# Optimization experiments

Measured on AMD Instinct MI355X. Metric: run time of the kernel, lower is better.

The kernel has to match this reference:

```python
import jax, jax.numpy as jnp
import numpy as np

N = 50000
E = 800000
C_IN = 32
C_OUT = 32
K = 8  # number of branch MLPs


def setup_inputs() -> dict:
    key = jax.random.key(0)
    ks = jax.random.split(key, 12)
    x = jax.random.normal(ks[0], (N, C_IN), dtype=jnp.float32)
    pos = jax.random.normal(ks[1], (N, 2), dtype=jnp.float32)
    edge_index = jax.random.randint(ks[2], (2, E), 0, N, dtype=jnp.int32)
    edge_attr = jax.random.normal(ks[3], (E, 4), dtype=jnp.float32)
    edge_weight = jax.random.uniform(ks[4], (E,), dtype=jnp.float32)
    s1 = 1.0 / np.sqrt(C_IN + 4)
    s2 = 1.0 / np.sqrt(C_OUT)
    W1 = jax.random.uniform(ks[5], (K, C_IN + 4, C_OUT), jnp.float32, -s1, s1)
    b1 = jax.random.uniform(ks[6], (K, C_OUT), jnp.float32, -s1, s1)
    W2 = jax.random.uniform(ks[7], (K, C_OUT, C_OUT), jnp.float32, -s2, s2)
    b2 = jax.random.uniform(ks[8], (K, C_OUT), jnp.float32, -s2, s2)
    sr = 1.0 / np.sqrt(C_IN)
    Wr = jax.random.uniform(ks[9], (C_IN, C_OUT), jnp.float32, -sr, sr)
    br = jax.random.uniform(ks[10], (C_OUT,), jnp.float32, -sr, sr)
    return {"x": x, "pos": pos, "edge_index": edge_index, "edge_attr": edge_attr,
            "edge_weight": edge_weight, "W1": W1, "b1": b1, "W2": W2, "b2": b2,
            "Wr": Wr, "br": br}


def reference(x, pos, edge_index, edge_attr, edge_weight, W1, b1, W2, b2, Wr, br):
    src = edge_index[0]  # j (source / neighbor)
    tgt = edge_index[1]  # i (target / aggregation index)

    # gather per-edge features
    x_i = x[tgt]                      # [E, C_IN]
    x_j = x[src]                      # [E, C_IN]
    diff = pos[src] - pos[tgt]        # [E, 2]

    # geometric branch index in [0, 8)
    con0 = (diff[:, 0] > 0).astype(jnp.int32)
    con1 = (diff[:, 1] > 0).astype(jnp.int32)
    con2 = (jnp.abs(diff[:, 0]) - jnp.abs(diff[:, 1]) > 0).astype(jnp.int32)
    idx = con0 + con1 * 2 + con2 * 4  # [E]

    m = jnp.concatenate([x_j - x_i, edge_attr], axis=1)  # [E, C_IN+4]
    # all 8 branch MLPs (Linear->ReLU->Linear->ReLU), then select per edge
    h = jax.nn.relu(jnp.einsum('ec,kcf->ekf', m, W1) + b1[None])   # [E, K, C_OUT]
    f_all = jax.nn.relu(jnp.einsum('ekf,kfg->ekg', h, W2) + b2[None])
    f = jnp.take_along_axis(f_all, idx[:, None, None], axis=1)[:, 0, :]  # [E, C_OUT]
    f = edge_weight[:, None] * f

    # scatter-mean over target nodes
    seg_sum = jax.ops.segment_sum(f, tgt, num_segments=N)
    counts = jax.ops.segment_sum(jnp.ones((f.shape[0],), f.dtype), tgt, num_segments=N)
    out = seg_sum / jnp.maximum(counts, 1.0)[:, None]

    # skip connection
    out = out + x @ Wr + br
    return out
```

## Files before the change

kernel.cpp:

```cpp
#include <hip/hip_runtime.h>

#define N_NODES 50000
#define N_EDGES 800000
#define K_BR    8
#define N_C     196
#define N_BUK   1568
#define CAP_SLOTS 898816
#define MLP_WAVES (CAP_SLOTS/64)
#define FATB    98

typedef _Float16 h2 __attribute__((ext_vector_type(2)));
typedef _Float16 half8 __attribute__((ext_vector_type(8)));
typedef float f32x4 __attribute__((ext_vector_type(4)));

#define MFMA(a, b, c) __builtin_amdgcn_mfma_f32_16x16x32_f16((a), (b), (c), 0, 0, 0)


__device__ __forceinline__ int branch_idx(float dx, float dy) {
    return (dx > 0.0f ? 1 : 0) + (dy > 0.0f ? 2 : 0) +
           ((fabsf(dx) - fabsf(dy)) > 0.0f ? 4 : 0);
}

__device__ __forceinline__ unsigned pk_f16pair(float a, float b) {
    h2 p; p.x = (_Float16)a; p.y = (_Float16)b;
    return __builtin_bit_cast(unsigned, p);
}

__device__ __forceinline__ unsigned short f16bits(float a) {
    _Float16 h = (_Float16)a;
    return __builtin_bit_cast(unsigned short, h);
}

__global__ void __launch_bounds__(1024) hist_kernel(
    const int* __restrict__ ei, const float* __restrict__ pos,
    const float* __restrict__ x,
    int* __restrict__ bucketCnt, unsigned short* __restrict__ kcArr,
    unsigned* __restrict__ xh) {
    __shared__ int h[N_BUK];
    int t = threadIdx.x;
    for (int j = t; j < N_BUK; j += 1024) h[j] = 0;
    __syncthreads();
#pragma unroll
    for (int i = 0; i < 8; ++i) {
        int e = blockIdx.x * 8192 + i * 1024 + t;
        if (e < N_EDGES) {
            int s = ei[e], d = ei[N_EDGES + e];
            float2 ps = ((const float2*)pos)[s];
            float2 pd = ((const float2*)pos)[d];
            int k = branch_idx(ps.x - pd.x, ps.y - pd.y);
            int b = k * N_C + (d >> 8);
            atomicAdd(&h[b], 1);
            kcArr[e] = (unsigned short)b;
            float2 xv = ((const float2*)x)[e];
            xh[e] = pk_f16pair(xv.x, xv.y);
        }
    }
    __syncthreads();
    for (int j = t; j < N_BUK; j += 1024) {
        int c = h[j];
        if (c) atomicAdd(&bucketCnt[j], c);
    }
}

__global__ void __launch_bounds__(1024) tiny_kernel(
    const int* __restrict__ bucketCnt, int* __restrict__ slotStart,
    int* __restrict__ binStart,
    const float* __restrict__ W1, const float* __restrict__ W2,
    uint4* __restrict__ w1f4, uint4* __restrict__ w2f4) {
    __shared__ int sc[1024];
    __shared__ int sb[256];
    int t = threadIdx.x;
    int b0 = 2 * t, b1 = 2 * t + 1;
    int a0 = (b0 < N_BUK) ? ((bucketCnt[b0] + 63) & ~63) : 0;
    int a1 = (b1 < N_BUK) ? ((bucketCnt[b1] + 63) & ~63) : 0;
    sc[t] = a0 + a1;
    __syncthreads();
    for (int off = 1; off < 1024; off <<= 1) {
        int tmp = (t >= off) ? sc[t - off] : 0;
        __syncthreads();
        sc[t] += tmp;
        __syncthreads();
    }
    int excl = sc[t] - (a0 + a1);
    if (b0 < N_BUK) slotStart[b0] = excl;
    if (b1 < N_BUK) slotStart[b1] = excl + a0;
    if (t == 1023) slotStart[N_BUK] = sc[1023];

    int v = 0;
    if (t < N_C) {
#pragma unroll
        for (int k = 0; k < K_BR; ++k) v += bucketCnt[k * N_C + t];
    }
    if (t < 256) sb[t] = v;
    __syncthreads();
    for (int off = 1; off < 256; off <<= 1) {
        int tmp = (t < 256 && t >= off) ? sb[t - off] : 0;
        __syncthreads();
        if (t < 256) sb[t] += tmp;
        __syncthreads();
    }
    if (t < N_C) binStart[t] = sb[t] - v;
    if (t == 255) binStart[N_C] = sb[255];

    for (int idx = t; idx < 3072; idx += 1024) {
        if (idx < 2048) {
            int L = idx & 63, fl = idx >> 6;
            int nt = fl & 1, kt = (fl >> 1) & 1, kk = fl >> 2;
            int quad = L >> 4, col = L & 15;
            unsigned dw[4];
#pragma unroll
            for (int i = 0; i < 4; ++i) {
                float v0 = 0.0f, v1 = 0.0f;
                int k0 = kt * 32 + quad * 8 + 2 * i;
                if (k0 < 36)     v0 = W1[kk * 1152 + k0 * 32 + nt * 16 + col];
                if (k0 + 1 < 36) v1 = W1[kk * 1152 + (k0 + 1) * 32 + nt * 16 + col];
                dw[i] = pk_f16pair(v0, v1);
            }
            w1f4[idx] = make_uint4(dw[0], dw[1], dw[2], dw[3]);
        } else {
            int u2 = idx - 2048;
            int L = u2 & 63, fl = u2 >> 6;
            int nt = fl & 1, kk = fl >> 1;
            int quad = L >> 4, col = L & 15;
            unsigned dw[4];
#pragma unroll
            for (int i = 0; i < 4; ++i) {
                int k0 = quad * 8 + 2 * i;
                dw[i] = pk_f16pair(W2[kk * 1024 + k0 * 32 + nt * 16 + col],
                                   W2[kk * 1024 + (k0 + 1) * 32 + nt * 16 + col]);
            }
            w2f4[u2] = make_uint4(dw[0], dw[1], dw[2], dw[3]);
        }
    }
}

__global__ void __launch_bounds__(1024) scatter_kernel(
    const int* __restrict__ ei, const float* __restrict__ ea,
    const float* __restrict__ ew, const unsigned short* __restrict__ kcArr,
    const int* __restrict__ slotStart, int* __restrict__ bucketCur,
    uint4* __restrict__ payload) {
    __shared__ int h[N_BUK];
    __shared__ int base[N_BUK];
    int t = threadIdx.x;
    for (int j = t; j < N_BUK; j += 1024) h[j] = 0;
    __syncthreads();
    unsigned sd[8], brk[8], e01[8], e23[8], ewh[8];
#pragma unroll
    for (int i = 0; i < 8; ++i) {
        int e = blockIdx.x * 8192 + i * 1024 + t;
        bool v = e < N_EDGES;
        int b = 0, rk = 0;
        if (v) {
            int s = ei[e], d = ei[N_EDGES + e];
            sd[i] = (unsigned)s | ((unsigned)d << 16);
            b = kcArr[e];
            rk = atomicAdd(&h[b], 1);
            float4 eav = ((const float4*)ea)[e];
            e01[i] = pk_f16pair(eav.x, eav.y);
            e23[i] = pk_f16pair(eav.z, eav.w);
            ewh[i] = (unsigned)f16bits(ew[e]);
        }
        brk[i] = (unsigned)b | ((unsigned)rk << 16) | (v ? 0x80000000u : 0u);
    }
    __syncthreads();
    for (int j = t; j < N_BUK; j += 1024) {
        int c = h[j];
        base[j] = c ? atomicAdd(&bucketCur[j], c) : 0;
    }
    __syncthreads();
#pragma unroll
    for (int i = 0; i < 8; ++i) {
        if (brk[i] & 0x80000000u) {
            int b = (int)(brk[i] & 0xFFFFu);
            int rk = (int)((brk[i] >> 16) & 0x7FFFu);
            int slot = slotStart[b] + base[b] + rk;
            payload[slot] = make_uint4(sd[i], ewh[i] << 16, e01[i], e23[i]);
        }
    }
}

__global__ void __launch_bounds__(1024) binsort_kernel(
    const uint4* __restrict__ payload, const int* __restrict__ slotStart,
    const int* __restrict__ bucketCnt, const int* __restrict__ binStart,
    int* __restrict__ slotOf, int* __restrict__ nodeStartG, int* __restrict__ degG) {
    __shared__ int cntA[256], cntB[256], startL[256], scn[256];
    int t = threadIdx.x, c = blockIdx.x;
    if (t < 256) { cntA[t] = 0; cntB[t] = 0; }
    __syncthreads();
    const unsigned* p32 = (const unsigned*)payload;
    for (int k = 0; k < K_BR; ++k) {
        int b = k * N_C + c, st = slotStart[b], rows = bucketCnt[b];
        for (int r = t; r < rows; r += 1024) {
            int n = (int)((p32[4 * (size_t)(st + r)] >> 16) & 255u);
            atomicAdd(&cntA[n], 1);
        }
    }
    __syncthreads();
    int v = (t < 256) ? cntA[t] : 0;
    if (t < 256) scn[t] = v;
    __syncthreads();
    for (int off = 1; off < 256; off <<= 1) {
        int tmp = (t < 256 && t >= off) ? scn[t - off] : 0;
        __syncthreads();
        if (t < 256) scn[t] += tmp;
        __syncthreads();
    }
    if (t < 256) startL[t] = scn[t] - v;
    __syncthreads();
    int bb = binStart[c];
    if (t < 256) {
        int g = c * 256 + t;
        if (g < N_NODES) { nodeStartG[g] = bb + startL[t]; degG[g] = v; }
    }
    for (int k = 0; k < K_BR; ++k) {
        int b = k * N_C + c, st = slotStart[b], rows = bucketCnt[b];
        for (int r = t; r < rows; r += 1024) {
            int slot = st + r;
            int n = (int)((p32[4 * (size_t)slot] >> 16) & 255u);
            int rk = atomicAdd(&cntB[n], 1);
            slotOf[slot] = bb + startL[n] + rk;
        }
    }
}

__global__ void __launch_bounds__(64) mlp_kernel(
    const uint4* __restrict__ payload,
    const unsigned* __restrict__ xh,
    const uint4* __restrict__ w1f4, const float* __restrict__ b1,
    const uint4* __restrict__ w2f4, const float* __restrict__ b2,
    const int* __restrict__ slotStart, const int* __restrict__ bucketCnt,
    const int* __restrict__ slotOf,
    unsigned short* __restrict__ fbuf) {
    __shared__ uint4 lds4[656];
    char* mreg = (char*)lds4;
    char* hreg = mreg + 9216;

    int u = __builtin_amdgcn_readfirstlane((int)blockIdx.x * 64);
    if (u >= slotStart[N_BUK]) return;
    int lo = 0;
#pragma unroll
    for (int st = 1024; st; st >>= 1) {
        int cand = lo + st;
        if (cand < N_BUK && slotStart[cand] <= u) lo = cand;
    }
    int b = __builtin_amdgcn_readfirstlane(lo);
    int fill = bucketCnt[b];
    int rel0 = u - slotStart[b];
    if (rel0 >= fill) return;
    int k = b / N_C;

    int L = threadIdx.x;
    int quad = L >> 4, col = L & 15;
    int slot = u + L;
    bool valid = (rel0 + L) < fill;

    uint4 pl = payload[slot];
    int so = slotOf[slot];
    int s = (int)(pl.x & 0xFFFFu);
    int d = (int)(pl.x >> 16);
    _Float16 wh = __builtin_bit_cast(_Float16, (unsigned short)(pl.y >> 16));

    const uint4* xj = ((const uint4*)xh) + 4 * (size_t)s;
    const uint4* xi = ((const uint4*)xh) + 4 * (size_t)d;
    uint4* mrow = (uint4*)(mreg + L * 144);
#pragma unroll
    for (int q = 0; q < 4; ++q) {
        half8 a8 = __builtin_bit_cast(half8, xj[q]);
        half8 b8 = __builtin_bit_cast(half8, xi[q]);
        half8 d8 = a8 - b8;
        mrow[q] = __builtin_bit_cast(uint4, d8);
    }
    mrow[4] = make_uint4(pl.z, pl.w, 0u, 0u);
    mrow[5] = make_uint4(0u, 0u, 0u, 0u);
    mrow[6] = make_uint4(0u, 0u, 0u, 0u);
    mrow[7] = make_uint4(0u, 0u, 0u, 0u);

    half8 B1[2][2], B2[2];
#pragma unroll
    for (int kt = 0; kt < 2; ++kt)
#pragma unroll
        for (int nt = 0; nt < 2; ++nt)
            B1[kt][nt] = __builtin_bit_cast(half8, w1f4[((k * 2 + kt) * 2 + nt) * 64 + L]);
#pragma unroll
    for (int nt = 0; nt < 2; ++nt)
        B2[nt] = __builtin_bit_cast(half8, w2f4[(k * 2 + nt) * 64 + L]);
    float b1o0 = b1[k * 32 + col],      b1o1 = b1[k * 32 + 16 + col];
    float b2o0 = b2[k * 32 + col],      b2o1 = b2[k * 32 + 16 + col];

#pragma unroll
    for (int mt = 0; mt < 4; ++mt) {
        int arow = mt * 16 + col;
        half8 a0 = __builtin_bit_cast(half8, *(const uint4*)(mreg + arow * 144 + quad * 16));
        half8 a1 = __builtin_bit_cast(half8, *(const uint4*)(mreg + arow * 144 + 64 + quad * 16));
        f32x4 c0 = {b1o0, b1o0, b1o0, b1o0};
        f32x4 c1 = {b1o1, b1o1, b1o1, b1o1};
        c0 = MFMA(a0, B1[0][0], c0);
        c0 = MFMA(a1, B1[1][0], c0);
        c1 = MFMA(a0, B1[0][1], c1);
        c1 = MFMA(a1, B1[1][1], c1);
#pragma unroll
        for (int r = 0; r < 4; ++r) {
            int er = quad * 4 + r;
            *(unsigned short*)(hreg + er * 80 + col * 2) =
                __builtin_bit_cast(unsigned short, (_Float16)fmaxf(c0[r], 0.0f));
            *(unsigned short*)(hreg + er * 80 + (16 + col) * 2) =
                __builtin_bit_cast(unsigned short, (_Float16)fmaxf(c1[r], 0.0f));
        }
        half8 ah = __builtin_bit_cast(half8, *(const uint4*)(hreg + col * 80 + quad * 16));
        f32x4 d0 = {b2o0, b2o0, b2o0, b2o0};
        f32x4 d1 = {b2o1, b2o1, b2o1, b2o1};
        d0 = MFMA(ah, B2[0], d0);
        d1 = MFMA(ah, B2[1], d1);
#pragma unroll
        for (int r = 0; r < 4; ++r) {
            int edge = mt * 16 + quad * 4 + r;
            *(unsigned short*)(mreg + edge * 144 + col * 2) =
                __builtin_bit_cast(unsigned short, (_Float16)fmaxf(d0[r], 0.0f));
            *(unsigned short*)(mreg + edge * 144 + (16 + col) * 2) =
                __builtin_bit_cast(unsigned short, (_Float16)fmaxf(d1[r], 0.0f));
        }
    }

    half8 w8 = {wh, wh, wh, wh, wh, wh, wh, wh};
    uint4* orow = (uint4*)(mreg + L * 144);
    uint4* frow = (uint4*)(fbuf + 32 * (size_t)so);
#pragma unroll
    for (int q = 0; q < 4; ++q) {
        half8 v8 = __builtin_bit_cast(half8, orow[q]);
        v8 = v8 * w8;
        if (valid) frow[q] = __builtin_bit_cast(uint4, v8);
    }
}

__global__ void agg_kernel(const unsigned short* __restrict__ fbuf,
                           const int* __restrict__ nodeStartG, const int* __restrict__ degG,
                           const float* __restrict__ x, const float* __restrict__ Wr,
                           const float* __restrict__ br, float* __restrict__ out) {
    int t = blockIdx.x * blockDim.x + threadIdx.x;
    if (t >= N_NODES * 8) return;
    int n = t >> 3, g8 = t & 7;
    int st = nodeStartG[n], dg = degG[n];
    const uint2* fb = (const uint2*)fbuf;
    float a0 = 0.0f, a1 = 0.0f, a2 = 0.0f, a3 = 0.0f;
    for (int j = 0; j < dg; ++j) {
        uint2 uu = fb[(size_t)(st + j) * 8 + g8];
        h2 p01 = __builtin_bit_cast(h2, uu.x);
        h2 p23 = __builtin_bit_cast(h2, uu.y);
        a0 += (float)p01.x;
        a1 += (float)p01.y;
        a2 += (float)p23.x;
        a3 += (float)p23.y;
    }
    float inv = 1.0f / (float)max(dg, 1);
    int o = g8 * 4;
    a0 = a0 * inv + br[o];
    a1 = a1 * inv + br[o + 1];
    a2 = a2 * inv + br[o + 2];
    a3 = a3 * inv + br[o + 3];
    const float* xr = x + 32 * (size_t)n;
#pragma unroll
    for (int c = 0; c < 32; ++c) {
        float xv = xr[c];
        a0 = fmaf(xv, Wr[c * 32 + o], a0);
        a1 = fmaf(xv, Wr[c * 32 + o + 1], a1);
        a2 = fmaf(xv, Wr[c * 32 + o + 2], a2);
        a3 = fmaf(xv, Wr[c * 32 + o + 3], a3);
    }
    float4* o4 = (float4*)(out + 32 * (size_t)n + o);
    *o4 = make_float4(a0, a1, a2, a3);
}

extern "C" void kernel_launch(void* const* d_in, const int* in_sizes, int n_in,
                              void* d_out, int out_size, void* d_ws, size_t ws_size,
                              hipStream_t stream) {
    const float* x   = (const float*)d_in[0];
    const float* pos = (const float*)d_in[1];
    const int*   ei  = (const int*)d_in[2];
    const float* ea  = (const float*)d_in[3];
    const float* ew  = (const float*)d_in[4];
    const float* W1  = (const float*)d_in[5];
    const float* b1  = (const float*)d_in[6];
    const float* W2  = (const float*)d_in[7];
    const float* b2  = (const float*)d_in[8];
    const float* Wr  = (const float*)d_in[9];
    const float* br  = (const float*)d_in[10];
    float* out = (float*)d_out;

    char* ws = (char*)d_ws;
    unsigned short* fbuf   = (unsigned short*)(ws + 0);
    uint4* payload         = (uint4*)(ws + 51200000);
    unsigned* xh           = (unsigned*)(ws + 65581056);
    unsigned short* kcArr  = (unsigned short*)(ws + 68781056);
    int* bucketCnt         = (int*)(ws + 70381056);
    int* bucketCur         = (int*)(ws + 70387328);
    int* slotStart         = (int*)(ws + 70393600);
    int* binStart          = (int*)(ws + 70399876);
    int* nodeStartG        = (int*)(ws + 70400664);
    int* degG              = (int*)(ws + 70600664);
    int* slotOf            = (int*)(ws + 70800664);
    uint4* w1f4            = (uint4*)(ws + 74395936);
    uint4* w2f4            = (uint4*)(ws + 74428704);

    hipMemsetAsync(bucketCnt, 0, 12544, stream);

    hist_kernel<<<FATB, 1024, 0, stream>>>(ei, pos, x, bucketCnt, kcArr, xh);
    tiny_kernel<<<1, 1024, 0, stream>>>(bucketCnt, slotStart, binStart, W1, W2, w1f4, w2f4);
    scatter_kernel<<<FATB, 1024, 0, stream>>>(ei, ea, ew, kcArr, slotStart,
                                              bucketCur, payload);
    binsort_kernel<<<N_C, 1024, 0, stream>>>(payload, slotStart, bucketCnt, binStart,
                                             slotOf, nodeStartG, degG);
    mlp_kernel<<<MLP_WAVES, 64, 0, stream>>>(payload, xh, w1f4, b1, w2f4, b2,
                                             slotStart, bucketCnt, slotOf, fbuf);
    agg_kernel<<<(N_NODES * 8 + 255) / 256, 256, 0, stream>>>(fbuf, nodeStartG, degG,
                                                              x, Wr, br, out);
}
```

Measured before the change: 203.4 us.

## Replace global bucket atomics with per-block histograms and deterministic prefix offsets

The histogram kernel now writes a per-block histogram row instead of atomically adding into global bucket counts. The single-block tiny kernel computes per-block base offsets with a serial scan over 196 blocks for each bucket. The scatter kernel then reads those precomputed bases instead of doing global atomics on a cursor array. Block count doubles, with half the edges per block, to raise occupancy. This drops the memset and the global atomic contention, but adds a serial 196-step loop per bucket in a one-block kernel plus extra workspace traffic.

Measured after the change: 210.1 us. 3.3% more time.

```diff
diff --git a/kernel.cpp b/kernel.cpp
--- a/kernel.cpp
+++ b/kernel.cpp
@@ -7,7 +7,7 @@
 #define N_BUK   1568
 #define CAP_SLOTS 898816
 #define MLP_WAVES (CAP_SLOTS/64)
-#define FATB    98
+#define EBLK    196
 
 typedef _Float16 h2 __attribute__((ext_vector_type(2)));
 typedef _Float16 half8 __attribute__((ext_vector_type(8)));
@@ -34,15 +34,15 @@
 __global__ void __launch_bounds__(1024) hist_kernel(
     const int* __restrict__ ei, const float* __restrict__ pos,
     const float* __restrict__ x,
-    int* __restrict__ bucketCnt, unsigned short* __restrict__ kcArr,
+    int* __restrict__ blockHist, unsigned short* __restrict__ kcArr,
     unsigned* __restrict__ xh) {
     __shared__ int h[N_BUK];
     int t = threadIdx.x;
     for (int j = t; j < N_BUK; j += 1024) h[j] = 0;
     __syncthreads();
 #pragma unroll
-    for (int i = 0; i < 8; ++i) {
-        int e = blockIdx.x * 8192 + i * 1024 + t;
+    for (int i = 0; i < 4; ++i) {
+        int e = blockIdx.x * 4096 + i * 1024 + t;
         if (e < N_EDGES) {
             int s = ei[e], d = ei[N_EDGES + e];
             float2 ps = ((const float2*)pos)[s];
@@ -56,23 +56,34 @@
         }
     }
     __syncthreads();
-    for (int j = t; j < N_BUK; j += 1024) {
-        int c = h[j];
-        if (c) atomicAdd(&bucketCnt[j], c);
-    }
+    int* row = blockHist + (size_t)blockIdx.x * N_BUK;
+    for (int j = t; j < N_BUK; j += 1024) row[j] = h[j];
 }
 
 __global__ void __launch_bounds__(1024) tiny_kernel(
-    const int* __restrict__ bucketCnt, int* __restrict__ slotStart,
+    const int* __restrict__ blockHist, int* __restrict__ blockBase,
+    int* __restrict__ bucketCnt, int* __restrict__ slotStart,
     int* __restrict__ binStart,
     const float* __restrict__ W1, const float* __restrict__ W2,
     uint4* __restrict__ w1f4, uint4* __restrict__ w2f4) {
     __shared__ int sc[1024];
     __shared__ int sb[256];
+    __shared__ int sbCnt[N_BUK];
     int t = threadIdx.x;
+    for (int b = t; b < N_BUK; b += 1024) {
+        int sum = 0;
+        for (int blk = 0; blk < EBLK; ++blk) {
+            size_t o = (size_t)blk * N_BUK + b;
+            blockBase[o] = sum;
+            sum += blockHist[o];
+        }
+        sbCnt[b] = sum;
+        bucketCnt[b] = sum;
+    }
+    __syncthreads();
     int b0 = 2 * t, b1 = 2 * t + 1;
-    int a0 = (b0 < N_BUK) ? ((bucketCnt[b0] + 63) & ~63) : 0;
-    int a1 = (b1 < N_BUK) ? ((bucketCnt[b1] + 63) & ~63) : 0;
+    int a0 = (b0 < N_BUK) ? ((sbCnt[b0] + 63) & ~63) : 0;
+    int a1 = (b1 < N_BUK) ? ((sbCnt[b1] + 63) & ~63) : 0;
     sc[t] = a0 + a1;
     __syncthreads();
     for (int off = 1; off < 1024; off <<= 1) {
@@ -89,7 +100,7 @@
     int v = 0;
     if (t < N_C) {
 #pragma unroll
-        for (int k = 0; k < K_BR; ++k) v += bucketCnt[k * N_C + t];
+        for (int k = 0; k < K_BR; ++k) v += sbCnt[k * N_C + t];
     }
     if (t < 256) sb[t] = v;
     __syncthreads();
@@ -137,17 +148,17 @@
 __global__ void __launch_bounds__(1024) scatter_kernel(
     const int* __restrict__ ei, const float* __restrict__ ea,
     const float* __restrict__ ew, const unsigned short* __restrict__ kcArr,
-    const int* __restrict__ slotStart, int* __restrict__ bucketCur,
+    const int* __restrict__ slotStart, const int* __restrict__ blockBase,
     uint4* __restrict__ payload) {
     __shared__ int h[N_BUK];
     __shared__ int base[N_BUK];
     int t = threadIdx.x;
     for (int j = t; j < N_BUK; j += 1024) h[j] = 0;
     __syncthreads();
-    unsigned sd[8], brk[8], e01[8], e23[8], ewh[8];
-#pragma unroll
-    for (int i = 0; i < 8; ++i) {
-        int e = blockIdx.x * 8192 + i * 1024 + t;
+    unsigned sd[4], brk[4], e01[4], e23[4], ewh[4];
+#pragma unroll
+    for (int i = 0; i < 4; ++i) {
+        int e = blockIdx.x * 4096 + i * 1024 + t;
         bool v = e < N_EDGES;
         int b = 0, rk = 0;
         if (v) {
@@ -163,18 +174,15 @@
         brk[i] = (unsigned)b | ((unsigned)rk << 16) | (v ? 0x80000000u : 0u);
     }
     __syncthreads();
-    for (int j = t; j < N_BUK; j += 1024) {
-        int c = h[j];
-        base[j] = c ? atomicAdd(&bucketCur[j], c) : 0;
-    }
-    __syncthreads();
-#pragma unroll
-    for (int i = 0; i < 8; ++i) {
+    const int* bb = blockBase + (size_t)blockIdx.x * N_BUK;
+    for (int j = t; j < N_BUK; j += 1024) base[j] = slotStart[j] + bb[j];
+    __syncthreads();
+#pragma unroll
+    for (int i = 0; i < 4; ++i) {
         if (brk[i] & 0x80000000u) {
             int b = (int)(brk[i] & 0xFFFFu);
             int rk = (int)((brk[i] >> 16) & 0x7FFFu);
-            int slot = slotStart[b] + base[b] + rk;
-            payload[slot] = make_uint4(sd[i], ewh[i] << 16, e01[i], e23[i]);
+            payload[base[b] + rk] = make_uint4(sd[i], ewh[i] << 16, e01[i], e23[i]);
         }
     }
 }
@@ -391,22 +399,22 @@
     uint4* payload         = (uint4*)(ws + 51200000);
     unsigned* xh           = (unsigned*)(ws + 65581056);
     unsigned short* kcArr  = (unsigned short*)(ws + 68781056);
-    int* bucketCnt         = (int*)(ws + 70381056);
-    int* bucketCur         = (int*)(ws + 70387328);
-    int* slotStart         = (int*)(ws + 70393600);
-    int* binStart          = (int*)(ws + 70399876);
-    int* nodeStartG        = (int*)(ws + 70400664);
-    int* degG              = (int*)(ws + 70600664);
-    int* slotOf            = (int*)(ws + 70800664);
-    uint4* w1f4            = (uint4*)(ws + 74395936);
-    uint4* w2f4            = (uint4*)(ws + 74428704);
-
-    hipMemsetAsync(bucketCnt, 0, 12544, stream);
-
-    hist_kernel<<<FATB, 1024, 0, stream>>>(ei, pos, x, bucketCnt, kcArr, xh);
-    tiny_kernel<<<1, 1024, 0, stream>>>(bucketCnt, slotStart, binStart, W1, W2, w1f4, w2f4);
-    scatter_kernel<<<FATB, 1024, 0, stream>>>(ei, ea, ew, kcArr, slotStart,
-                                              bucketCur, payload);
+    int* blockHist         = (int*)(ws + 70381056);
+    int* blockBase         = (int*)(ws + 71610368);
+    int* bucketCnt         = (int*)(ws + 72839680);
+    int* slotStart         = (int*)(ws + 72845952);
+    int* binStart          = (int*)(ws + 72852228);
+    int* nodeStartG        = (int*)(ws + 72853016);
+    int* degG              = (int*)(ws + 73053016);
+    int* slotOf            = (int*)(ws + 73253016);
+    uint4* w1f4            = (uint4*)(ws + 76848288);
+    uint4* w2f4            = (uint4*)(ws + 76881056);
+
+    hist_kernel<<<EBLK, 1024, 0, stream>>>(ei, pos, x, blockHist, kcArr, xh);
+    tiny_kernel<<<1, 1024, 0, stream>>>(blockHist, blockBase, bucketCnt, slotStart,
+                                        binStart, W1, W2, w1f4, w2f4);
+    scatter_kernel<<<EBLK, 1024, 0, stream>>>(ei, ea, ew, kcArr, slotStart,
+                                              blockBase, payload);
     binsort_kernel<<<N_C, 1024, 0, stream>>>(payload, slotStart, bucketCnt, binStart,
                                              slotOf, nodeStartG, degG);
     mlp_kernel<<<MLP_WAVES, 64, 0, stream>>>(payload, xh, w1f4, b1, w2f4, b2,
```
